# Optimization experiments

Hardware: AMD Instinct MI355X
Metric: run time of the kernel (lower is better)

Reference implementation:

```python
import jax, jax.numpy as jnp
import numpy as np
from jax import lax

N, K, T_OBS, PRED = 64, 48, 30, 15
EMB, NODE, EDGE, ATT, CNN = 64, 128, 256, 64, 512


def setup_inputs():
    key = jax.random.key(0)
    ks = jax.random.split(key, 18)
    rn = lambda k, s, sc=1.0: jax.random.normal(k, s, jnp.float32) * sc
    return {
        "img_embedding": rn(ks[0], (N, CNN)),
        "target_obs_pos_abs": rn(ks[1], (N, T_OBS, 2)),
        "target_obs_pos_rel": rn(ks[2], (N, T_OBS, 2)),
        "target_obs_pos_step": rn(ks[3], (N, T_OBS, 2), 0.1),
        "nearby_obs_pos_abs": rn(ks[4], (N, K, T_OBS, 2)),
        "nearby_obs_pos_rel": rn(ks[5], (N, K, T_OBS, 2)),
        "nearby_obs_pos_step": rn(ks[6], (N, K, T_OBS, 2), 0.1),
        "target_obs_hist_size": jax.random.randint(ks[7], (N, 1), 0, T_OBS),
        "nearby_obs_hist_sizes": jax.random.randint(ks[8], (N, K, 1), 0, T_OBS),
        "W_disp": rn(ks[9], (EMB, 2), 0.1), "b_disp": jnp.zeros((EMB,), jnp.float32),
        "Wih_t": rn(ks[10], (4 * NODE, EMB), 0.05), "Whh_t": rn(ks[11], (4 * NODE, NODE), 0.05),
        "bih_t": jnp.zeros((4 * NODE,), jnp.float32), "bhh_t": jnp.zeros((4 * NODE,), jnp.float32),
        "Wih_n": rn(ks[12], (4 * EDGE, EMB), 0.05), "Whh_n": rn(ks[13], (4 * EDGE, EDGE), 0.05),
        "bih_n": jnp.zeros((4 * EDGE,), jnp.float32), "bhh_n": jnp.zeros((4 * EDGE,), jnp.float32),
        "W_att_t": rn(ks[14], (ATT, 2), 0.1), "b_att_t": jnp.zeros((ATT,), jnp.float32),
        "W_att_n": rn(ks[15], (ATT, 2), 0.1), "b_att_n": jnp.zeros((ATT,), jnp.float32),
        "W_pred": rn(ks[16], (2, NODE + CNN + EDGE), 0.02), "b_pred": jnp.zeros((2,), jnp.float32),
    }


def _lstm_cell(x, h, c, Wih, Whh, bih, bhh):
    # PyTorch LSTM gate order: i, f, g, o
    g = x @ Wih.T + h @ Whh.T + bih + bhh
    i, f, gg, o = jnp.split(g, 4, axis=-1)
    c2 = jax.nn.sigmoid(f) * c + jax.nn.sigmoid(i) * jnp.tanh(gg)
    return jax.nn.sigmoid(o) * jnp.tanh(c2), c2


def _forward(img_embedding, target_obs_pos_abs, target_obs_pos_rel, target_obs_pos_step,
             nearby_obs_pos_abs, nearby_obs_pos_rel, nearby_obs_pos_step,
             W_disp, b_disp, Wih_t, Whh_t, bih_t, bhh_t, Wih_n, Whh_n, bih_n, bhh_n,
             W_att_t, b_att_t, W_att_n, b_att_n, W_pred, b_pred,
             target_obs_hist_size, nearby_obs_hist_sizes):
    t_hist = target_obs_hist_size[:, 0]          # [N]
    n_hist = nearby_obs_hist_sizes[:, :, 0]      # [N, K]
    M = N * K

    def step(carry, t):
        tht, tct, nht, nct, Ht, cabs, crel, cstep, nabs, nstep = carry
        is_obs = t < T_OBS
        tc = jnp.minimum(t, T_OBS - 1)
        # prediction branch (only takes effect when t >= T_OBS)
        pred_out = jnp.concatenate([tht, img_embedding, Ht], 1) @ W_pred.T + b_pred  # [N,2]
        cabs = jnp.where(is_obs, target_obs_pos_abs[:, tc], cabs + pred_out)
        crel = jnp.where(is_obs, target_obs_pos_rel[:, tc], crel + pred_out)
        cstep = jnp.where(is_obs, target_obs_pos_step[:, tc], pred_out)
        nabs = jnp.where(is_obs, nearby_obs_pos_abs[:, :, tc], nabs)
        nstep = jnp.where(is_obs, nearby_obs_pos_step[:, :, tc], nstep)
        tmask = jnp.where(is_obs, t_hist > T_OBS - t, True)   # [N] bool
        nmask = jnp.where(is_obs, n_hist > T_OBS - t, True)   # [N,K] bool
        gate_t = jnp.sum(tmask) > 0  # emulates 'continue' when no target observed
        # target LSTM step, masked scatter-back
        th2, tc2 = _lstm_cell(cstep @ W_disp.T + b_disp, tht, tct, Wih_t, Whh_t, bih_t, bhh_t)
        u = (tmask & gate_t)[:, None]
        tht = jnp.where(u, th2, tht)
        tct = jnp.where(u, tc2, tct)
        # nearby LSTM step, masked scatter-back
        currN = jnp.sum(nmask)
        gate_n = gate_t & (currN > 0)
        nh2, nc2 = _lstm_cell(nstep.reshape(M, 2) @ W_disp.T + b_disp, nht, nct, Wih_n, Whh_n, bih_n, bhh_n)
        un = (nmask.reshape(M) & gate_n)[:, None]
        nht = jnp.where(un, nh2, nht)
        nct = jnp.where(un, nc2, nct)
        # social attention over padded nearby dim
        an = (nabs - cabs[:, None, :]) @ W_att_n.T + b_att_n   # [N,K,ATT]
        at = crel @ W_att_t.T + b_att_t                        # [N,ATT]
        mf = nmask.astype(jnp.float32)
        sc = jnp.einsum('nka,na->nk', an, at) * currN.astype(jnp.float32) / jnp.sqrt(jnp.float32(ATT))
        sc = sc * mf
        num = jnp.exp(sc - jnp.max(sc, 1, keepdims=True)) * mf
        w = num / (jnp.sum(num, 1, keepdims=True) + 1e-6)
        Ht = jnp.where(gate_n, jnp.einsum('nke,nk->ne', nht.reshape(N, K, EDGE), w), Ht)
        return (tht, tct, nht, nct, Ht, cabs, crel, cstep, nabs, nstep), crel

    z = lambda s: jnp.zeros(s, jnp.float32)
    init = (z((N, NODE)), z((N, NODE)), z((M, EDGE)), z((M, EDGE)), z((N, EDGE)),
            z((N, 2)), z((N, 2)), z((N, 2)), z((N, K, 2)), z((N, K, 2)))
    _, rels = lax.scan(step, init, jnp.arange(1, T_OBS + PRED))
    # last PRED emitted crel values are pred_traj[:, 0:PRED]
    return jnp.transpose(rels[-PRED:], (1, 0, 2))


def reference(img_embedding, target_obs_pos_abs, target_obs_pos_rel, target_obs_pos_step,
              nearby_obs_pos_abs, nearby_obs_pos_rel, nearby_obs_pos_step,
              target_obs_hist_size, nearby_obs_hist_sizes,
              W_disp, b_disp, Wih_t, Whh_t, bih_t, bhh_t, Wih_n, Whh_n, bih_n, bhh_n,
              W_att_t, b_att_t, W_att_n, b_att_n, W_pred, b_pred):
    return _forward(img_embedding, target_obs_pos_abs, target_obs_pos_rel, target_obs_pos_step,
                    nearby_obs_pos_abs, nearby_obs_pos_rel, nearby_obs_pos_step,
                    W_disp, b_disp, Wih_t, Whh_t, bih_t, bhh_t, Wih_n, Whh_n, bih_n, bhh_n,
                    W_att_t, b_att_t, W_att_n, b_att_n, W_pred, b_pred,
                    target_obs_hist_size, nearby_obs_hist_sizes)
```

## Files before the change

kernel.cpp:

```cpp
#include <hip/hip_runtime.h>
#include <math.h>

#define NT 64
#define KN 48
#define TOBS 30
#define NPRED 15
#define EMB 64
#define NODE 128
#define EDGE 256
#define ATTD 64
#define CNN 512
#define GNN 1024
#define GTT 512
#define TMAX 44

typedef _Float16 f16;
typedef f16 f16x8 __attribute__((ext_vector_type(8)));
typedef f16 f16x2 __attribute__((ext_vector_type(2)));
typedef float f32x4 __attribute__((ext_vector_type(4)));

__device__ __forceinline__ float rcp_f(float x) { return __builtin_amdgcn_rcpf(x); }
__device__ __forceinline__ float sigm(float x) { return rcp_f(1.f + __expf(-x)); }
__device__ __forceinline__ float tanh_f(float x) {
  float xx = fminf(fmaxf(x, -20.f), 20.f);
  float e = __expf(-2.f * xx);
  return (1.f - e) * rcp_f(1.f + e);
}
__device__ __forceinline__ unsigned ldcoh(const unsigned* p) {
  return __hip_atomic_load(p, __ATOMIC_RELAXED, __HIP_MEMORY_SCOPE_AGENT);
}
__device__ __forceinline__ unsigned long long ldcoh8(const unsigned long long* p) {
  return __hip_atomic_load(p, __ATOMIC_RELAXED, __HIP_MEMORY_SCOPE_AGENT);
}
__device__ __forceinline__ float ldcohf(const float* p) {
  unsigned u = __hip_atomic_load((const unsigned*)p, __ATOMIC_RELAXED, __HIP_MEMORY_SCOPE_AGENT);
  return __builtin_bit_cast(float, u);
}
__device__ __forceinline__ void stcoh(unsigned* p, unsigned v) {
  __hip_atomic_store(p, v, __ATOMIC_RELAXED, __HIP_MEMORY_SCOPE_AGENT);
}
__device__ __forceinline__ void stcohf(float* p, float v) {
  __hip_atomic_store((unsigned*)p, __builtin_bit_cast(unsigned, v),
                     __ATOMIC_RELAXED, __HIP_MEMORY_SCOPE_AGENT);
}

__global__ __launch_bounds__(512) void prep_kernel(
    const float* __restrict__ Wih_n, const float* __restrict__ Whh_n,
    const float* __restrict__ bih_n, const float* __restrict__ bhh_n,
    const float* __restrict__ Wih_t, const float* __restrict__ Whh_t,
    const float* __restrict__ bih_t, const float* __restrict__ bhh_t,
    const float* __restrict__ W_disp, const float* __restrict__ b_disp,
    const int* __restrict__ t_hist, const int* __restrict__ n_hist,
    f16* __restrict__ Wn, f16* __restrict__ Wt,
    float* __restrict__ Ptv, float* __restrict__ Pnv,
    float* __restrict__ bias_n, float* __restrict__ bias_t,
    int* __restrict__ gt_arr, int* __restrict__ gn_arr, float* __restrict__ cn_arr,
    int* __restrict__ last29p, unsigned* __restrict__ flags)
{
  const int gid = blockIdx.x * 512 + threadIdx.x;
  const int nthr = gridDim.x * 512;
  __shared__ int sgn[TMAX + 1];

  if (gid < 2 * NT) flags[gid] = 0u;

  for (int idx = gid; idx < GNN * 288; idx += nthr) {
    const int j    = idx & 7;
    const int lane = (idx >> 3) & 63;
    const int g    = (idx >> 9) & 3;
    const int r    = idx >> 11;
    const int u    = r % 9;
    const int s    = r / 9;
    const int w    = s & 7;
    const int h    = s >> 3;
    const int col = g * 256 + h * 128 + w * 16 + (lane & 15);
    float v = 0.f;
    if (u > 0) {
      const int k = (u - 1) * 32 + (lane >> 4) * 8 + j;
      v = Whh_n[col * EDGE + k];
    }
    Wn[idx] = (f16)v;
  }
  for (int idx = gid; idx < GTT * 192; idx += nthr) {
    const int j = idx & 7;
    const int col = (idx >> 3) & 511;
    const int c8 = idx >> 12;
    const int k = c8 * 8 + j;
    const float v = (k < EMB) ? Wih_t[col * EMB + k] : Whh_t[col * NODE + (k - EMB)];
    Wt[idx] = (f16)v;
  }
  for (int idx = gid; idx < 3 * GTT; idx += nthr) {
    const int sel = idx / GTT;
    const int col = idx - sel * GTT;
    float acc = 0.f;
    for (int e = 0; e < EMB; ++e) {
      const float sv = (sel == 0) ? W_disp[e * 2]
                     : (sel == 1) ? W_disp[e * 2 + 1] : b_disp[e];
      acc += sv * Wih_t[col * EMB + e];
    }
    Ptv[sel * GTT + col] = acc;
  }
  for (int idx = gid; idx < 3 * GNN; idx += nthr) {
    const int sel = idx / GNN;
    const int col = idx - sel * GNN;
    float acc = 0.f;
    for (int e = 0; e < EMB; ++e) {
      const float sv = (sel == 0) ? W_disp[e * 2]
                     : (sel == 1) ? W_disp[e * 2 + 1] : b_disp[e];
      acc += sv * Wih_n[col * EMB + e];
    }
    Pnv[sel * GNN + col] = acc;
  }
  for (int idx = gid; idx < GNN; idx += nthr) bias_n[idx] = bih_n[idx] + bhh_n[idx];
  for (int idx = gid; idx < GTT; idx += nthr) bias_t[idx] = bih_t[idx] + bhh_t[idx];

  if (blockIdx.x == 0 && threadIdx.x < 352) {
    const int t = (threadIdx.x >> 3) + 1;
    const int part = threadIdx.x & 7;
    int any_t = 0, cnt = 0;
    if (t < TOBS) {
      const int thr = TOBS - t;
      for (int nn = part; nn < NT; nn += 8) any_t |= (t_hist[nn] > thr) ? 1 : 0;
      for (int m = part; m < NT * KN; m += 8) cnt += (n_hist[m] > thr) ? 1 : 0;
    } else { any_t = (part == 0); cnt = (part == 0) ? NT * KN : 0; }
    #pragma unroll
    for (int off = 1; off < 8; off <<= 1) {
      any_t |= __shfl_xor(any_t, off);
      cnt   += __shfl_xor(cnt, off);
    }
    if (part == 0) {
      const int gn = (any_t && cnt > 0) ? 1 : 0;
      gt_arr[t] = any_t;
      gn_arr[t] = gn;
      cn_arr[t] = (float)cnt;
      sgn[t] = gn;
    }
  }
  __syncthreads();
  if (blockIdx.x == 0 && threadIdx.x == 0) {
    int l = 30;
    for (int t = 29; t >= 1; --t) if (sgn[t]) { l = t; break; }
    last29p[0] = l;
  }
}

__global__ __launch_bounds__(512, 2) void model_kernel(
    const float* __restrict__ img, const float* __restrict__ tabs,
    const float* __restrict__ trel, const float* __restrict__ tstep,
    const float* __restrict__ nabs_g, const float* __restrict__ nstep_g,
    const int* __restrict__ thist_g, const int* __restrict__ nhist_g,
    const float* __restrict__ W_att_t, const float* __restrict__ b_att_t,
    const float* __restrict__ W_att_n, const float* __restrict__ b_att_n,
    const float* __restrict__ W_pred, const float* __restrict__ b_pred,
    const f16* __restrict__ Wn, const f16* __restrict__ Wt,
    const float* __restrict__ Ptv, const float* __restrict__ Pnv,
    const float* __restrict__ bias_n, const float* __restrict__ bias_t,
    const int* __restrict__ gt_arr, const int* __restrict__ gn_arr,
    const float* __restrict__ cn_arr, const int* __restrict__ last29p,
    unsigned* __restrict__ flags, unsigned* __restrict__ Hglob,
    float* __restrict__ Tglob,
    float* __restrict__ out)
{
  __shared__ f16 s_wlds[3 * 16384];
  __shared__ float s_step[KN][2];
  __shared__ f16 Ah[KN][264];
  __shared__ float s_tht[NODE];
  __shared__ float s_tct[64];
  __shared__ f16  s_th16[NODE];
  __shared__ float s_Ht[EDGE];
  __shared__ float s_g[256];
  __shared__ float s_bt[256];
  __shared__ float s_w[KN];
  __shared__ float s_scal[8];
  __shared__ float s_dd[4];
  __shared__ float s_pimg[2];
  __shared__ int   s_nh[KN];
  __shared__ float s_wp[2][384];
  __shared__ float s_wan0[ATTD], s_wan1[ATTD], s_ban[ATTD];
  __shared__ float s_wat0[ATTD], s_wat1[ATTD], s_bat[ATTD];

  const int tid  = threadIdx.x;
  const int n    = blockIdx.x & 63;
  const int hb   = blockIdx.x >> 6;
  const int w    = tid >> 6;
  const int lane = tid & 63;
  const int cl   = lane & 15;
  const int kq   = lane >> 4;
  const int koff = kq * 8;

  for (int i = tid; i < KN * 264; i += 512) ((f16*)Ah)[i] = (f16)0.f;
  if (tid < KN * 2) ((float*)s_step)[tid] = 0.f;
  for (int i = tid; i < NODE; i += 512) { s_tht[i] = 0.f; s_th16[i] = (f16)0.f; }
  if (tid < 64) s_tct[tid] = 0.f;
  for (int i = tid; i < EDGE; i += 512) s_Ht[i] = 0.f;
  if (tid < 256) {
    const int g = tid >> 6, dl = tid & 63;
    s_bt[tid] = bias_t[g * 128 + hb * 64 + dl];
  }
  for (int i = tid; i < 768; i += 512) {
    const int ww = i / 384, j = i - ww * 384;
    s_wp[ww][j] = (j < 128) ? W_pred[ww * 896 + j] : W_pred[ww * 896 + 640 + (j - 128)];
  }
  if (tid < KN) s_nh[tid] = nhist_g[n * KN + tid];
  if (tid < 8) s_scal[tid] = 0.f;
  if (tid >= 64 && tid < 128) {
    const int a = tid - 64;
    s_wan0[a] = W_att_n[a * 2]; s_wan1[a] = W_att_n[a * 2 + 1]; s_ban[a] = b_att_n[a];
  }
  if (tid >= 128 && tid < 192) {
    const int a = tid - 128;
    s_wat0[a] = W_att_t[a * 2]; s_wat1[a] = W_att_t[a * 2 + 1]; s_bat[a] = b_att_t[a];
  }
  const int thist = thist_g[n];
  const int last29 = last29p[0];

  float pt0 = 0.f, pt1 = 0.f, ptb = 0.f;
  if (tid < 256) {
    const int col = (tid >> 6) * 128 + hb * 64 + (tid & 63);
    pt0 = Ptv[col]; pt1 = Ptv[512 + col]; ptb = Ptv[1024 + col];
  }

  const int e_g = hb * 128 + w * 16 + cl;

  float pn0[4], pn1[4], bias_q[4];
  #pragma unroll
  for (int g = 0; g < 4; ++g) {
    const int col = g * 256 + e_g;
    pn0[g] = Pnv[col];
    pn1[g] = Pnv[1024 + col];
    bias_q[g] = bias_n[col] + Pnv[2048 + col];
  }

  for (int i = tid; i < 3 * 8 * 256; i += 512) {
    const int c  = i & 255;
    const int wv = (i >> 8) & 7;
    const int sl = i >> 11;
    const size_t gbase = ((size_t)((hb * 8 + wv) * 9 + (sl + 1))) * 2048;
    *(f16x8*)(s_wlds + (size_t)(sl * 8 + wv) * 2048 + c * 8) =
        *(const f16x8*)(Wn + gbase + c * 8);
  }

  if (w < 2) {
    float s = 0.f;
    for (int j = lane; j < CNN; j += 64) s += img[n * CNN + j] * W_pred[w * 896 + 128 + j];
    for (int off = 32; off; off >>= 1) s += __shfl_down(s, off);
    if (lane == 0) s_pimg[w] = s + b_pred[w];
  }

  float creg[3][4];
  #pragma unroll
  for (int b = 0; b < 3; ++b)
    #pragma unroll
    for (int c = 0; c < 4; ++c) creg[b][c] = 0.f;

  const f16* gW = Wn + ((size_t)(hb * 8 + w) * 9) * 2048 + (size_t)lane * 8;
  const f16* lW = s_wlds + (size_t)w * 2048 + (size_t)lane * 8;
  unsigned* myflag = flags + n * 2 + hb;
  unsigned* otflag = flags + n * 2 + (1 - hb);
  int bn = 0;

  __syncthreads();

  {
    if (tid < 96) {
      const int row = tid >> 1, comp = tid & 1;
      s_step[row][comp] = nstep_g[((n * KN + row) * TOBS + 1) * 2 + comp];
    }
    if (tid < 2) {
      s_scal[tid]     = tabs[(n * TOBS + 1) * 2 + tid];
      s_scal[2 + tid] = trel[(n * TOBS + 1) * 2 + tid];
      s_scal[4 + tid] = tstep[(n * TOBS + 1) * 2 + tid];
    }
    if (tid >= 384 && tid < 448) {
      const int a = tid - 384;
      const float r0 = trel[(n * TOBS + 1) * 2 + 0], r1 = trel[(n * TOBS + 1) * 2 + 1];
      const float at = r0 * s_wat0[a] + r1 * s_wat1[a] + s_bat[a];
      float p0 = at * s_wan0[a], p1 = at * s_wan1[a], pb = at * s_ban[a];
      #pragma unroll
      for (int off = 32; off; off >>= 1) {
        p0 += __shfl_xor(p0, off); p1 += __shfl_xor(p1, off); pb += __shfl_xor(pb, off);
      }
      if (a == 0) { s_dd[0] = p0; s_dd[1] = p1; s_dd[2] = pb; }
    }
  }
  __syncthreads();

  for (int t = 1; t <= TMAX; ++t) {
    const bool is_obs = (t < TOBS);
    const int tc = is_obs ? t : (TOBS - 1);
    const int gate_t = gt_arr[t];
    const int gate_n = gn_arr[t];
    const float currN = cn_arr[t];
    const bool tmask = is_obs ? (thist > (TOBS - t)) : true;
    const bool do_t = gate_t && tmask;
    const bool need_x = (gate_n || do_t);
    const bool do_att = gate_n && (t >= last29);
    const int par = bn & 1;

    if (!is_obs) {
      if (w < 2) {
        float s = 0.f;
        for (int j = lane; j < NODE; j += 64) s += s_tht[j] * s_wp[w][j];
        for (int j = lane; j < EDGE; j += 64) s += s_Ht[j] * s_wp[w][128 + j];
        for (int off = 32; off; off >>= 1) s += __shfl_down(s, off);
        if (lane == 0) {
          const float p = s + s_pimg[w];
          const float cabs = s_scal[w] + p;
          const float crel = s_scal[2 + w] + p;
          s_scal[w] = cabs; s_scal[2 + w] = crel; s_scal[4 + w] = p;
          if (hb == 0) out[(n * NPRED + (t - TOBS)) * 2 + w] = crel;
        }
      }
      __syncthreads();
      if (tid >= 384 && tid < 448) {
        const int a = tid - 384;
        const float at = s_scal[2] * s_wat0[a] + s_scal[3] * s_wat1[a] + s_bat[a];
        float p0 = at * s_wan0[a], p1 = at * s_wan1[a], pb = at * s_ban[a];
        #pragma unroll
        for (int off = 32; off; off >>= 1) {
          p0 += __shfl_xor(p0, off); p1 += __shfl_xor(p1, off); pb += __shfl_xor(pb, off);
        }
        if (a == 0) { s_dd[0] = p0; s_dd[1] = p1; s_dd[2] = pb; }
      }
      __syncthreads();
    }

    f16 hreg[3][4];
    if (gate_n) {
      f32x4 acc[3][4];
      #pragma unroll
      for (int rt = 0; rt < 3; ++rt)
        #pragma unroll
        for (int g = 0; g < 4; ++g) acc[rt][g] = (f32x4){0.f, 0.f, 0.f, 0.f};

      #pragma unroll
      for (int u = 1; u <= 8; ++u) {
        f16x8 bf[4];
        if (u <= 3) {
          #pragma unroll
          for (int g = 0; g < 4; ++g)
            bf[g] = *(const f16x8*)(lW + (u - 1) * 16384 + g * 512);
        } else {
          #pragma unroll
          for (int g = 0; g < 4; ++g)
            bf[g] = *(const f16x8*)(gW + u * 2048 + g * 512);
        }
        f16x8 af[3];
        #pragma unroll
        for (int rt = 0; rt < 3; ++rt) {
          const int row = rt * 16 + cl;
          af[rt] = *(const f16x8*)&Ah[row][(u - 1) * 32 + koff];
        }
        #pragma unroll
        for (int g = 0; g < 4; ++g)
          #pragma unroll
          for (int rt = 0; rt < 3; ++rt)
            acc[rt][g] = __builtin_amdgcn_mfma_f32_16x16x32_f16(af[rt], bf[g], acc[rt][g], 0, 0, 0);
      }

      unsigned* Hg = Hglob + (size_t)(par * NT + n) * (KN * 128);
      #pragma unroll
      for (int rt = 0; rt < 3; ++rt) {
        #pragma unroll
        for (int jj = 0; jj < 4; ++jj) {
          const int row = rt * 16 + kq * 4 + jj;
          const bool nm = is_obs ? (s_nh[row] > (TOBS - t)) : true;
          f16 hv;
          if (nm) {
            const float s0 = s_step[row][0], s1 = s_step[row][1];
            const float iv = acc[rt][0][jj] + bias_q[0] + s0 * pn0[0] + s1 * pn1[0];
            const float fv = acc[rt][1][jj] + bias_q[1] + s0 * pn0[1] + s1 * pn1[1];
            const float gv = acc[rt][2][jj] + bias_q[2] + s0 * pn0[2] + s1 * pn1[2];
            const float ov = acc[rt][3][jj] + bias_q[3] + s0 * pn0[3] + s1 * pn1[3];
            const float c2 = sigm(fv) * creg[rt][jj] + sigm(iv) * tanh_f(gv);
            creg[rt][jj] = c2;
            hv = (f16)(sigm(ov) * tanh_f(c2));
          } else {
            hv = Ah[row][e_g];
          }
          hreg[rt][jj] = hv;
          const unsigned lo = (unsigned)__builtin_bit_cast(unsigned short, hv);
          const unsigned hi = (unsigned)__shfl_down((int)lo, 1);
          if (!(cl & 1))
            stcoh(Hg + row * 128 + (e_g >> 1), lo | (hi << 16));
        }
      }
    }

    if (do_t && tid < 256) {
      float g0 = s_bt[tid] + s_scal[4] * pt0 + s_scal[5] * pt1 + ptb;
      float g1 = 0.f, g2 = 0.f, g3 = 0.f;
      const f16x2* th2 = (const f16x2*)s_th16;
      const f16x8* wp = (const f16x8*)(Wt + ((tid >> 6) * 128 + hb * 64 + (tid & 63)) * 8);
      #pragma unroll
      for (int c8 = 0; c8 < 16; ++c8) {
        const f16x8 wv = wp[(c8 + 8) * 512];
        f16x2 w0 = {wv[0], wv[1]}, w1 = {wv[2], wv[3]};
        f16x2 w2 = {wv[4], wv[5]}, w3 = {wv[6], wv[7]};
        g0 = __builtin_amdgcn_fdot2(w0, th2[c8 * 4 + 0], g0, false);
        g1 = __builtin_amdgcn_fdot2(w1, th2[c8 * 4 + 1], g1, false);
        g2 = __builtin_amdgcn_fdot2(w2, th2[c8 * 4 + 2], g2, false);
        g3 = __builtin_amdgcn_fdot2(w3, th2[c8 * 4 + 3], g3, false);
      }
      s_g[tid] = (g0 + g1) + (g2 + g3);
    }
    float screg = -1.0e30f, mfreg = 0.f;
    if (do_att && w == 4 && lane < KN) {
      const float a0 = nabs_g[((n * KN + lane) * TOBS + tc) * 2 + 0] - s_scal[0];
      const float a1 = nabs_g[((n * KN + lane) * TOBS + tc) * 2 + 1] - s_scal[1];
      const bool nm = is_obs ? (s_nh[lane] > (TOBS - t)) : true;
      screg = nm ? (a0 * s_dd[0] + a1 * s_dd[1] + s_dd[2]) * currN * 0.125f : 0.f;
      mfreg = nm ? 1.f : 0.f;
    }
    __syncthreads();

    if (do_t && tid < 64) {
      const int d = hb * 64 + tid;
      const float iv = s_g[tid], fv = s_g[64 + tid];
      const float gv = s_g[128 + tid], ov = s_g[192 + tid];
      const float c2 = sigm(fv) * s_tct[tid] + sigm(iv) * tanh_f(gv);
      s_tct[tid] = c2;
      const float nh = sigm(ov) * tanh_f(c2);
      s_tht[d] = nh;
      s_th16[d] = (f16)nh;
      stcohf(Tglob + ((size_t)(par * NT + n) * 2 + hb) * 64 + tid, nh);
    }
    if (w == 0) {
      asm volatile("s_waitcnt vmcnt(0)" ::: "memory");
      if (need_x && lane == 0) stcoh(myflag, (unsigned)(bn + 1));
    }
    if (do_att && w == 4) {
      float mx = screg;
      #pragma unroll
      for (int off = 32; off; off >>= 1) mx = fmaxf(mx, __shfl_xor(mx, off));
      float num = __expf(screg - mx) * mfreg;
      float sum = num;
      #pragma unroll
      for (int off = 32; off; off >>= 1) sum += __shfl_xor(sum, off);
      if (lane < KN) s_w[lane] = num * rcp_f(sum + 1e-6f);
    }

    if (gate_n) {
      #pragma unroll
      for (int rt = 0; rt < 3; ++rt)
        #pragma unroll
        for (int jj = 0; jj < 4; ++jj)
          Ah[rt * 16 + kq * 4 + jj][e_g] = hreg[rt][jj];
    }

    if (need_x) {
      if (lane == 0) {
        const unsigned step = (unsigned)(bn + 1);
        while (ldcoh(otflag) < step)
          __builtin_amdgcn_s_sleep(1);
      }
    }
    unsigned long long pv0 = 0, pv1 = 0, pv2 = 0;
    float tpull = 0.f;
    const int pr = tid >> 5, pc = tid & 31;
    if (gate_n) {
      const unsigned long long* Hg8 =
          (const unsigned long long*)(Hglob + (size_t)(par * NT + n) * (KN * 128));
      const int ob8 = (1 - hb) * 32;
      pv0 = ldcoh8(Hg8 + (pr)      * 64 + ob8 + pc);
      pv1 = ldcoh8(Hg8 + (pr + 16) * 64 + ob8 + pc);
      pv2 = ldcoh8(Hg8 + (pr + 32) * 64 + ob8 + pc);
    }
    if (do_t && tid >= 448) {
      tpull = ldcohf(Tglob + ((size_t)(par * NT + n) * 2 + (1 - hb)) * 64 + (tid - 448));
    }

    {
      const int tn = t + 1;
      if (tn <= TOBS) {
        const int tcn = (tn < TOBS) ? tn : (TOBS - 1);
        if (tid < 96) {
          const int row = tid >> 1, comp = tid & 1;
          s_step[row][comp] = nstep_g[((n * KN + row) * TOBS + tcn) * 2 + comp];
        }
      }
      if (tn < TOBS) {
        if (tid < 2) {
          s_scal[tid]     = tabs[(n * TOBS + tn) * 2 + tid];
          s_scal[2 + tid] = trel[(n * TOBS + tn) * 2 + tid];
          s_scal[4 + tid] = tstep[(n * TOBS + tn) * 2 + tid];
        }
        if (tid >= 384 && tid < 448) {
          const int a = tid - 384;
          const float r0 = trel[(n * TOBS + tn) * 2 + 0], r1 = trel[(n * TOBS + tn) * 2 + 1];
          const float at = r0 * s_wat0[a] + r1 * s_wat1[a] + s_bat[a];
          float p0 = at * s_wan0[a], p1 = at * s_wan1[a], pb = at * s_ban[a];
          #pragma unroll
          for (int off = 32; off; off >>= 1) {
            p0 += __shfl_xor(p0, off); p1 += __shfl_xor(p1, off); pb += __shfl_xor(pb, off);
          }
          if (a == 0) { s_dd[0] = p0; s_dd[1] = p1; s_dd[2] = pb; }
        }
      }
    }

    if (gate_n) {
      const int cb = ((1 - hb) * 64 + pc * 2) * 2;
      *(unsigned long long*)&Ah[pr][cb]      = pv0;
      *(unsigned long long*)&Ah[pr + 16][cb] = pv1;
      *(unsigned long long*)&Ah[pr + 32][cb] = pv2;
    }
    if (do_t && tid >= 448) {
      const int d = (1 - hb) * 64 + (tid - 448);
      s_tht[d] = tpull;
      s_th16[d] = (f16)tpull;
    }
    __syncthreads();

    if (do_att && tid < EDGE) {
      float h0 = 0.f, h1 = 0.f, h2 = 0.f, h3 = 0.f;
      #pragma unroll
      for (int k = 0; k < KN; k += 4) {
        h0 += (float)Ah[k][tid]     * s_w[k];
        h1 += (float)Ah[k + 1][tid] * s_w[k + 1];
        h2 += (float)Ah[k + 2][tid] * s_w[k + 2];
        h3 += (float)Ah[k + 3][tid] * s_w[k + 3];
      }
      s_Ht[tid] = (h0 + h1) + (h2 + h3);
    }
    if (need_x) bn++;
    if (t >= 29) __syncthreads();
  }
}

extern "C" void kernel_launch(void* const* d_in, const int* in_sizes, int n_in,
                              void* d_out, int out_size, void* d_ws, size_t ws_size,
                              hipStream_t stream) {
  const float* img    = (const float*)d_in[0];
  const float* tabs   = (const float*)d_in[1];
  const float* trel   = (const float*)d_in[2];
  const float* tstep  = (const float*)d_in[3];
  const float* nabs   = (const float*)d_in[4];
  const float* nstep  = (const float*)d_in[6];
  const int*   thist  = (const int*)d_in[7];
  const int*   nhist  = (const int*)d_in[8];
  const float* W_disp = (const float*)d_in[9];
  const float* b_disp = (const float*)d_in[10];
  const float* Wih_t  = (const float*)d_in[11];
  const float* Whh_t  = (const float*)d_in[12];
  const float* bih_t  = (const float*)d_in[13];
  const float* bhh_t  = (const float*)d_in[14];
  const float* Wih_n  = (const float*)d_in[15];
  const float* Whh_n  = (const float*)d_in[16];
  const float* bih_n  = (const float*)d_in[17];
  const float* bhh_n  = (const float*)d_in[18];
  const float* W_att_t = (const float*)d_in[19];
  const float* b_att_t = (const float*)d_in[20];
  const float* W_att_n = (const float*)d_in[21];
  const float* b_att_n = (const float*)d_in[22];
  const float* W_pred  = (const float*)d_in[23];
  const float* b_pred  = (const float*)d_in[24];

  char* ws = (char*)d_ws;
  f16*      Wn      = (f16*)(ws);
  f16*      Wt      = (f16*)(ws + 655360);
  float*    bias_n  = (float*)(ws + 851968);
  float*    bias_t  = (float*)(ws + 856064);
  int*      gt_arr  = (int*)(ws + 858112);
  int*      gn_arr  = (int*)(ws + 858304);
  float*    cn_arr  = (float*)(ws + 858496);
  int*      last29p = (int*)(ws + 859648);
  unsigned* flags   = (unsigned*)(ws + 860160);
  float*    Ptv     = (float*)(ws + 901120);
  float*    Pnv     = (float*)(ws + 917504);
  unsigned* Hglob   = (unsigned*)(ws + 1048576);
  float*    Tglob   = (float*)(ws + 4194304);

  prep_kernel<<<64, 512, 0, stream>>>(Wih_n, Whh_n, bih_n, bhh_n, Wih_t, Whh_t,
                                      bih_t, bhh_t, W_disp, b_disp,
                                      thist, nhist, Wn, Wt, Ptv, Pnv,
                                      bias_n, bias_t, gt_arr, gn_arr, cn_arr,
                                      last29p, flags);
  model_kernel<<<2 * NT, 512, 0, stream>>>(img, tabs, trel, tstep, nabs, nstep,
                                           thist, nhist,
                                           W_att_t, b_att_t, W_att_n, b_att_n,
                                           W_pred, b_pred,
                                           Wn, Wt, Ptv, Pnv, bias_n, bias_t,
                                           gt_arr, gn_arr, cn_arr, last29p,
                                           flags, Hglob, Tglob,
                                           (float*)d_out);
}
```

Baseline: 613.0 us.

## Merge paired per-sample blocks into one 1024-thread block, removing cross-block exchange

Before, each sample was split across two 512-thread blocks that swapped LSTM hidden-state halves through global memory with flag spin-waits every step. Now one 1024-thread block handles a whole sample, so the exchange becomes a __syncthreads plus LDS, and the global stores, flag polling and pulls are gone. The trade-off is that only one of the eight weight slices per wave now fits in LDS (16 groups × 1 slice, versus 3 slices before), so more Whh_n fragments stream from global/L2 each step. Only 64 blocks run, which halves the number of CUs in use.

```diff
diff --git a/kernel.cpp b/kernel.cpp
--- a/kernel.cpp
+++ b/kernel.cpp
@@ -25,23 +25,6 @@
   float xx = fminf(fmaxf(x, -20.f), 20.f);
   float e = __expf(-2.f * xx);
   return (1.f - e) * rcp_f(1.f + e);
-}
-__device__ __forceinline__ unsigned ldcoh(const unsigned* p) {
-  return __hip_atomic_load(p, __ATOMIC_RELAXED, __HIP_MEMORY_SCOPE_AGENT);
-}
-__device__ __forceinline__ unsigned long long ldcoh8(const unsigned long long* p) {
-  return __hip_atomic_load(p, __ATOMIC_RELAXED, __HIP_MEMORY_SCOPE_AGENT);
-}
-__device__ __forceinline__ float ldcohf(const float* p) {
-  unsigned u = __hip_atomic_load((const unsigned*)p, __ATOMIC_RELAXED, __HIP_MEMORY_SCOPE_AGENT);
-  return __builtin_bit_cast(float, u);
-}
-__device__ __forceinline__ void stcoh(unsigned* p, unsigned v) {
-  __hip_atomic_store(p, v, __ATOMIC_RELAXED, __HIP_MEMORY_SCOPE_AGENT);
-}
-__device__ __forceinline__ void stcohf(float* p, float v) {
-  __hip_atomic_store((unsigned*)p, __builtin_bit_cast(unsigned, v),
-                     __ATOMIC_RELAXED, __HIP_MEMORY_SCOPE_AGENT);
 }
 
 __global__ __launch_bounds__(512) void prep_kernel(
@@ -143,7 +126,7 @@
   }
 }
 
-__global__ __launch_bounds__(512, 2) void model_kernel(
+__global__ __launch_bounds__(1024, 1) void model_kernel(
     const float* __restrict__ img, const float* __restrict__ tabs,
     const float* __restrict__ trel, const float* __restrict__ tstep,
     const float* __restrict__ nabs_g, const float* __restrict__ nstep_g,
@@ -156,19 +139,17 @@
     const float* __restrict__ bias_n, const float* __restrict__ bias_t,
     const int* __restrict__ gt_arr, const int* __restrict__ gn_arr,
     const float* __restrict__ cn_arr, const int* __restrict__ last29p,
-    unsigned* __restrict__ flags, unsigned* __restrict__ Hglob,
-    float* __restrict__ Tglob,
     float* __restrict__ out)
 {
-  __shared__ f16 s_wlds[3 * 16384];
+  __shared__ f16 s_wlds[16 * 2048];
   __shared__ float s_step[KN][2];
   __shared__ f16 Ah[KN][264];
   __shared__ float s_tht[NODE];
-  __shared__ float s_tct[64];
+  __shared__ float s_tct[NODE];
   __shared__ f16  s_th16[NODE];
   __shared__ float s_Ht[EDGE];
-  __shared__ float s_g[256];
-  __shared__ float s_bt[256];
+  __shared__ float s_g[512];
+  __shared__ float s_bt[512];
   __shared__ float s_w[KN];
   __shared__ float s_scal[8];
   __shared__ float s_dd[4];
@@ -179,24 +160,22 @@
   __shared__ float s_wat0[ATTD], s_wat1[ATTD], s_bat[ATTD];
 
   const int tid  = threadIdx.x;
-  const int n    = blockIdx.x & 63;
-  const int hb   = blockIdx.x >> 6;
+  const int n    = blockIdx.x;
   const int w    = tid >> 6;
   const int lane = tid & 63;
   const int cl   = lane & 15;
   const int kq   = lane >> 4;
   const int koff = kq * 8;
-
-  for (int i = tid; i < KN * 264; i += 512) ((f16*)Ah)[i] = (f16)0.f;
+  const int e_g  = ((w >> 3) * 128) + ((w & 7) * 16) + cl;
+
+  for (int i = tid; i < KN * 264; i += 1024) ((f16*)Ah)[i] = (f16)0.f;
   if (tid < KN * 2) ((float*)s_step)[tid] = 0.f;
-  for (int i = tid; i < NODE; i += 512) { s_tht[i] = 0.f; s_th16[i] = (f16)0.f; }
-  if (tid < 64) s_tct[tid] = 0.f;
-  for (int i = tid; i < EDGE; i += 512) s_Ht[i] = 0.f;
-  if (tid < 256) {
-    const int g = tid >> 6, dl = tid & 63;
-    s_bt[tid] = bias_t[g * 128 + hb * 64 + dl];
-  }
-  for (int i = tid; i < 768; i += 512) {
+  for (int i = tid; i < NODE; i += 1024) {
+    s_tht[i] = 0.f; s_tct[i] = 0.f; s_th16[i] = (f16)0.f;
+  }
+  for (int i = tid; i < EDGE; i += 1024) s_Ht[i] = 0.f;
+  if (tid < 512) s_bt[tid] = bias_t[tid];
+  for (int i = tid; i < 768; i += 1024) {
     const int ww = i / 384, j = i - ww * 384;
     s_wp[ww][j] = (j < 128) ? W_pred[ww * 896 + j] : W_pred[ww * 896 + 640 + (j - 128)];
   }
@@ -214,12 +193,9 @@
   const int last29 = last29p[0];
 
   float pt0 = 0.f, pt1 = 0.f, ptb = 0.f;
-  if (tid < 256) {
-    const int col = (tid >> 6) * 128 + hb * 64 + (tid & 63);
-    pt0 = Ptv[col]; pt1 = Ptv[512 + col]; ptb = Ptv[1024 + col];
-  }
-
-  const int e_g = hb * 128 + w * 16 + cl;
+  if (tid < 512) {
+    pt0 = Ptv[tid]; pt1 = Ptv[512 + tid]; ptb = Ptv[1024 + tid];
+  }
 
   float pn0[4], pn1[4], bias_q[4];
   #pragma unroll
@@ -230,12 +206,11 @@
     bias_q[g] = bias_n[col] + Pnv[2048 + col];
   }
 
-  for (int i = tid; i < 3 * 8 * 256; i += 512) {
-    const int c  = i & 255;
-    const int wv = (i >> 8) & 7;
-    const int sl = i >> 11;
-    const size_t gbase = ((size_t)((hb * 8 + wv) * 9 + (sl + 1))) * 2048;
-    *(f16x8*)(s_wlds + (size_t)(sl * 8 + wv) * 2048 + c * 8) =
+  for (int i = tid; i < 16 * 256; i += 1024) {
+    const int c   = i & 255;
+    const int grp = i >> 8;
+    const size_t gbase = ((size_t)(grp * 9 + 1)) * 2048;
+    *(f16x8*)(s_wlds + (size_t)grp * 2048 + c * 8) =
         *(const f16x8*)(Wn + gbase + c * 8);
   }
 
@@ -252,11 +227,8 @@
     #pragma unroll
     for (int c = 0; c < 4; ++c) creg[b][c] = 0.f;
 
-  const f16* gW = Wn + ((size_t)(hb * 8 + w) * 9) * 2048 + (size_t)lane * 8;
+  const f16* gW = Wn + ((size_t)(w * 9)) * 2048 + (size_t)lane * 8;
   const f16* lW = s_wlds + (size_t)w * 2048 + (size_t)lane * 8;
-  unsigned* myflag = flags + n * 2 + hb;
-  unsigned* otflag = flags + n * 2 + (1 - hb);
-  int bn = 0;
 
   __syncthreads();
 
@@ -292,9 +264,7 @@
     const float currN = cn_arr[t];
     const bool tmask = is_obs ? (thist > (TOBS - t)) : true;
     const bool do_t = gate_t && tmask;
-    const bool need_x = (gate_n || do_t);
     const bool do_att = gate_n && (t >= last29);
-    const int par = bn & 1;
 
     if (!is_obs) {
       if (w < 2) {
@@ -307,7 +277,7 @@
           const float cabs = s_scal[w] + p;
           const float crel = s_scal[2 + w] + p;
           s_scal[w] = cabs; s_scal[2 + w] = crel; s_scal[4 + w] = p;
-          if (hb == 0) out[(n * NPRED + (t - TOBS)) * 2 + w] = crel;
+          out[(n * NPRED + (t - TOBS)) * 2 + w] = crel;
         }
       }
       __syncthreads();
@@ -335,10 +305,10 @@
       #pragma unroll
       for (int u = 1; u <= 8; ++u) {
         f16x8 bf[4];
-        if (u <= 3) {
+        if (u == 1) {
           #pragma unroll
           for (int g = 0; g < 4; ++g)
-            bf[g] = *(const f16x8*)(lW + (u - 1) * 16384 + g * 512);
+            bf[g] = *(const f16x8*)(lW + g * 512);
         } else {
           #pragma unroll
           for (int g = 0; g < 4; ++g)
@@ -357,14 +327,12 @@
             acc[rt][g] = __builtin_amdgcn_mfma_f32_16x16x32_f16(af[rt], bf[g], acc[rt][g], 0, 0, 0);
       }
 
-      unsigned* Hg = Hglob + (size_t)(par * NT + n) * (KN * 128);
       #pragma unroll
       for (int rt = 0; rt < 3; ++rt) {
         #pragma unroll
         for (int jj = 0; jj < 4; ++jj) {
           const int row = rt * 16 + kq * 4 + jj;
           const bool nm = is_obs ? (s_nh[row] > (TOBS - t)) : true;
-          f16 hv;
           if (nm) {
             const float s0 = s_step[row][0], s1 = s_step[row][1];
             const float iv = acc[rt][0][jj] + bias_q[0] + s0 * pn0[0] + s1 * pn1[0];
@@ -373,24 +341,19 @@
             const float ov = acc[rt][3][jj] + bias_q[3] + s0 * pn0[3] + s1 * pn1[3];
             const float c2 = sigm(fv) * creg[rt][jj] + sigm(iv) * tanh_f(gv);
             creg[rt][jj] = c2;
-            hv = (f16)(sigm(ov) * tanh_f(c2));
+            hreg[rt][jj] = (f16)(sigm(ov) * tanh_f(c2));
           } else {
-            hv = Ah[row][e_g];
+            hreg[rt][jj] = Ah[row][e_g];
           }
-          hreg[rt][jj] = hv;
-          const unsigned lo = (unsigned)__builtin_bit_cast(unsigned short, hv);
-          const unsigned hi = (unsigned)__shfl_down((int)lo, 1);
-          if (!(cl & 1))
-            stcoh(Hg + row * 128 + (e_g >> 1), lo | (hi << 16));
-        }
-      }
-    }
-
-    if (do_t && tid < 256) {
+        }
+      }
+    }
+
+    if (do_t && tid < 512) {
       float g0 = s_bt[tid] + s_scal[4] * pt0 + s_scal[5] * pt1 + ptb;
       float g1 = 0.f, g2 = 0.f, g3 = 0.f;
       const f16x2* th2 = (const f16x2*)s_th16;
-      const f16x8* wp = (const f16x8*)(Wt + ((tid >> 6) * 128 + hb * 64 + (tid & 63)) * 8);
+      const f16x8* wp = (const f16x8*)Wt + tid;
       #pragma unroll
       for (int c8 = 0; c8 < 16; ++c8) {
         const f16x8 wv = wp[(c8 + 8) * 512];
@@ -403,42 +366,35 @@
       }
       s_g[tid] = (g0 + g1) + (g2 + g3);
     }
-    float screg = -1.0e30f, mfreg = 0.f;
-    if (do_att && w == 4 && lane < KN) {
-      const float a0 = nabs_g[((n * KN + lane) * TOBS + tc) * 2 + 0] - s_scal[0];
-      const float a1 = nabs_g[((n * KN + lane) * TOBS + tc) * 2 + 1] - s_scal[1];
-      const bool nm = is_obs ? (s_nh[lane] > (TOBS - t)) : true;
-      screg = nm ? (a0 * s_dd[0] + a1 * s_dd[1] + s_dd[2]) * currN * 0.125f : 0.f;
-      mfreg = nm ? 1.f : 0.f;
+    if (do_att && w == 8) {
+      float sc = -1.0e30f, mf = 0.f;
+      if (lane < KN) {
+        const float a0 = nabs_g[((n * KN + lane) * TOBS + tc) * 2 + 0] - s_scal[0];
+        const float a1 = nabs_g[((n * KN + lane) * TOBS + tc) * 2 + 1] - s_scal[1];
+        const bool nm = is_obs ? (s_nh[lane] > (TOBS - t)) : true;
+        sc = nm ? (a0 * s_dd[0] + a1 * s_dd[1] + s_dd[2]) * currN * 0.125f : 0.f;
+        mf = nm ? 1.f : 0.f;
+      }
+      float mx = sc;
+      #pragma unroll
+      for (int off = 32; off; off >>= 1) mx = fmaxf(mx, __shfl_xor(mx, off));
+      float num = __expf(sc - mx) * mf;
+      float sum = num;
+      #pragma unroll
+      for (int off = 32; off; off >>= 1) sum += __shfl_xor(sum, off);
+      if (lane < KN) s_w[lane] = num * rcp_f(sum + 1e-6f);
     }
     __syncthreads();
 
-    if (do_t && tid < 64) {
-      const int d = hb * 64 + tid;
-      const float iv = s_g[tid], fv = s_g[64 + tid];
-      const float gv = s_g[128 + tid], ov = s_g[192 + tid];
+    if (do_t && tid < NODE) {
+      const float iv = s_g[tid], fv = s_g[128 + tid];
+      const float gv = s_g[256 + tid], ov = s_g[384 + tid];
       const float c2 = sigm(fv) * s_tct[tid] + sigm(iv) * tanh_f(gv);
       s_tct[tid] = c2;
       const float nh = sigm(ov) * tanh_f(c2);
-      s_tht[d] = nh;
-      s_th16[d] = (f16)nh;
-      stcohf(Tglob + ((size_t)(par * NT + n) * 2 + hb) * 64 + tid, nh);
-    }
-    if (w == 0) {
-      asm volatile("s_waitcnt vmcnt(0)" ::: "memory");
-      if (need_x && lane == 0) stcoh(myflag, (unsigned)(bn + 1));
-    }
-    if (do_att && w == 4) {
-      float mx = screg;
-      #pragma unroll
-      for (int off = 32; off; off >>= 1) mx = fmaxf(mx, __shfl_xor(mx, off));
-      float num = __expf(screg - mx) * mfreg;
-      float sum = num;
-      #pragma unroll
-      for (int off = 32; off; off >>= 1) sum += __shfl_xor(sum, off);
-      if (lane < KN) s_w[lane] = num * rcp_f(sum + 1e-6f);
-    }
-
+      s_tht[tid] = nh;
+      s_th16[tid] = (f16)nh;
+    }
     if (gate_n) {
       #pragma unroll
       for (int rt = 0; rt < 3; ++rt)
@@ -446,29 +402,6 @@
         for (int jj = 0; jj < 4; ++jj)
           Ah[rt * 16 + kq * 4 + jj][e_g] = hreg[rt][jj];
     }
-
-    if (need_x) {
-      if (lane == 0) {
-        const unsigned step = (unsigned)(bn + 1);
-        while (ldcoh(otflag) < step)
-          __builtin_amdgcn_s_sleep(1);
-      }
-    }
-    unsigned long long pv0 = 0, pv1 = 0, pv2 = 0;
-    float tpull = 0.f;
-    const int pr = tid >> 5, pc = tid & 31;
-    if (gate_n) {
-      const unsigned long long* Hg8 =
-          (const unsigned long long*)(Hglob + (size_t)(par * NT + n) * (KN * 128));
-      const int ob8 = (1 - hb) * 32;
-      pv0 = ldcoh8(Hg8 + (pr)      * 64 + ob8 + pc);
-      pv1 = ldcoh8(Hg8 + (pr + 16) * 64 + ob8 + pc);
-      pv2 = ldcoh8(Hg8 + (pr + 32) * 64 + ob8 + pc);
-    }
-    if (do_t && tid >= 448) {
-      tpull = ldcohf(Tglob + ((size_t)(par * NT + n) * 2 + (1 - hb)) * 64 + (tid - 448));
-    }
-
     {
       const int tn = t + 1;
       if (tn <= TOBS) {
@@ -497,18 +430,6 @@
         }
       }
     }
-
-    if (gate_n) {
-      const int cb = ((1 - hb) * 64 + pc * 2) * 2;
-      *(unsigned long long*)&Ah[pr][cb]      = pv0;
-      *(unsigned long long*)&Ah[pr + 16][cb] = pv1;
-      *(unsigned long long*)&Ah[pr + 32][cb] = pv2;
-    }
-    if (do_t && tid >= 448) {
-      const int d = (1 - hb) * 64 + (tid - 448);
-      s_tht[d] = tpull;
-      s_th16[d] = (f16)tpull;
-    }
     __syncthreads();
 
     if (do_att && tid < EDGE) {
@@ -522,7 +443,6 @@
       }
       s_Ht[tid] = (h0 + h1) + (h2 + h3);
     }
-    if (need_x) bn++;
     if (t >= 29) __syncthreads();
   }
 }
@@ -567,20 +487,17 @@
   unsigned* flags   = (unsigned*)(ws + 860160);
   float*    Ptv     = (float*)(ws + 901120);
   float*    Pnv     = (float*)(ws + 917504);
-  unsigned* Hglob   = (unsigned*)(ws + 1048576);
-  float*    Tglob   = (float*)(ws + 4194304);
 
   prep_kernel<<<64, 512, 0, stream>>>(Wih_n, Whh_n, bih_n, bhh_n, Wih_t, Whh_t,
                                       bih_t, bhh_t, W_disp, b_disp,
                                       thist, nhist, Wn, Wt, Ptv, Pnv,
                                       bias_n, bias_t, gt_arr, gn_arr, cn_arr,
                                       last29p, flags);
-  model_kernel<<<2 * NT, 512, 0, stream>>>(img, tabs, trel, tstep, nabs, nstep,
-                                           thist, nhist,
-                                           W_att_t, b_att_t, W_att_n, b_att_n,
-                                           W_pred, b_pred,
-                                           Wn, Wt, Ptv, Pnv, bias_n, bias_t,
-                                           gt_arr, gn_arr, cn_arr, last29p,
-                                           flags, Hglob, Tglob,
-                                           (float*)d_out);
+  model_kernel<<<NT, 1024, 0, stream>>>(img, tabs, trel, tstep, nabs, nstep,
+                                        thist, nhist,
+                                        W_att_t, b_att_t, W_att_n, b_att_n,
+                                        W_pred, b_pred,
+                                        Wn, Wt, Ptv, Pnv, bias_n, bias_t,
+                                        gt_arr, gn_arr, cn_arr, last29p,
+                                        (float*)d_out);
 }
```

Result: slower. 990.5 us (+61.6%).
